# Performance work log

Hardware: AMD Instinct MI355X
Metric: run time of the kernel (lower is better)

## Reference

```python
import jax, jax.numpy as jnp
import numpy as np

B, D, P, C = 4096, 512, 256, 8
LAMBDA = 1.0


def setup_inputs() -> dict:
    key = jax.random.key(0)
    k1, k2, k3, k4 = jax.random.split(key, 4)
    x = jax.random.normal(k1, (B, D), dtype=jnp.float32)
    y = jax.random.randint(k2, (B,), 0, C, dtype=jnp.int32)
    prototypes = jax.random.normal(k3, (P, D), dtype=jnp.float32)
    # omega initialized as eye + 0.01*randn per class, like the torch module
    omega = jnp.eye(D, dtype=jnp.float32)[None] + 0.01 * jax.random.normal(k4, (C, D, D), dtype=jnp.float32)
    prototype_labels = (jnp.arange(P, dtype=jnp.int32) % C).astype(jnp.int32)
    return {"x": x, "y": y, "prototypes": prototypes, "omega": omega, "prototype_labels": prototype_labels}


def reference(x, y, prototypes, omega, prototype_labels):
    # transformed inputs per class: tx[c,b,:] = omega[c] @ x[b]
    tx = jnp.einsum('cij,bj->cbi', omega, x)                     # [C,B,D]
    # transformed prototypes under every class omega, then pick each
    # prototype's own class matrix: tp[p,:] = omega[label[p]] @ w[p]
    tp_all = jnp.einsum('cij,pj->cpi', omega, prototypes)        # [C,P,D]
    tp = tp_all[prototype_labels, jnp.arange(P)]                 # [P,D]
    # squared distances via expansion ||a-b||^2 = |a|^2 + |b|^2 - 2ab
    dots = jnp.einsum('cbd,pd->cbp', tx, tp)                     # [C,B,P]
    x2 = jnp.sum(tx * tx, axis=-1)                               # [C,B]
    p2 = jnp.sum(tp * tp, axis=-1)                               # [P]
    dist_all = x2[:, :, None] + p2[None, None, :] - 2.0 * dots   # [C,B,P]
    # each prototype uses the omega of its own class
    dist = dist_all[prototype_labels, :, jnp.arange(P)].T        # [B,P]
    same = prototype_labels[None, :] == y[:, None]               # [B,P]
    inf = jnp.float32(jnp.inf)
    pos = jnp.min(jnp.where(same, dist, inf), axis=1)            # [B]
    neg = jnp.min(jnp.where(same, inf, dist), axis=1)            # [B]
    mu = (pos - neg) / (pos + neg)
    loss = jnp.mean(jax.nn.sigmoid(LAMBDA * mu))
    loss = loss + 0.01 * jnp.linalg.norm(omega.reshape(-1))
    return loss
```

## Files before the change

### kernel.cpp

```cpp
#include <hip/hip_runtime.h>
#include <math.h>

typedef unsigned short ushort_t;
typedef __attribute__((ext_vector_type(8))) short short8;
typedef __attribute__((ext_vector_type(4))) float f32x4;

#define B_N 4096
#define D_N 512
#define P_N 256
#define C_N 8

#define ACC_OFF   0
#define P2G_OFF   256
#define X2_OFF    1280
#define XB_OFF    132352
#define OMB_OFF   (XB_OFF + B_N*D_N*2)
#define TPG_OFF   (OMB_OFF + C_N*D_N*D_N*2)
#define UG_OFF    (TPG_OFF + P_N*D_N*2)
#define OMBT_OFF  (UG_OFF + P_N*D_N*2)
#define MINB_OFF  OMBT_OFF

#define MFMA16(a, b, c) __builtin_amdgcn_mfma_f32_16x16x32_bf16(a, b, c, 0, 0, 0)

__device__ inline ushort_t f2bf(float f) {
    union { float f; unsigned u; } v; v.f = f;
    unsigned r = v.u + 0x7FFFu + ((v.u >> 16) & 1u);
    return (ushort_t)(r >> 16);
}

__device__ __forceinline__ void gll16(const ushort_t* g, ushort_t* l) {
    __builtin_amdgcn_global_load_lds((const __attribute__((address_space(1))) void*)g,
                                     (__attribute__((address_space(3))) void*)l, 16, 0, 0);
}

__global__ void k_cast(const float* __restrict__ x, const float* __restrict__ omega,
                       ushort_t* __restrict__ xb, ushort_t* __restrict__ omb,
                       ushort_t* __restrict__ ombT, float* __restrict__ oss) {
    __shared__ ushort_t T[64][72];
    __shared__ float red[4];
    int t = threadIdx.x;
    if (blockIdx.x < 1024) {
        int idx = blockIdx.x * 256 + t;
        const float4* x4 = (const float4*)x;
        float4 a = x4[idx * 2], b = x4[idx * 2 + 1];
        union { ushort_t s[8]; uint4 v; } o;
        o.s[0] = f2bf(a.x); o.s[1] = f2bf(a.y); o.s[2] = f2bf(a.z); o.s[3] = f2bf(a.w);
        o.s[4] = f2bf(b.x); o.s[5] = f2bf(b.y); o.s[6] = f2bf(b.z); o.s[7] = f2bf(b.w);
        ((uint4*)xb)[idx] = o.v;
        return;
    }
    int bid = blockIdx.x - 1024;
    int c = bid >> 6, by = (bid >> 3) & 7, bx = bid & 7;
    int r0 = by * 64, c0 = bx * 64;
    int r = t >> 2, seg = t & 3;
    const float* src = omega + ((size_t)c * D_N + r0 + r) * D_N + c0 + seg * 16;
    float4 v0 = ((const float4*)src)[0], v1 = ((const float4*)src)[1];
    float4 v2 = ((const float4*)src)[2], v3 = ((const float4*)src)[3];
    float s = v0.x*v0.x + v0.y*v0.y + v0.z*v0.z + v0.w*v0.w
            + v1.x*v1.x + v1.y*v1.y + v1.z*v1.z + v1.w*v1.w
            + v2.x*v2.x + v2.y*v2.y + v2.z*v2.z + v2.w*v2.w
            + v3.x*v3.x + v3.y*v3.y + v3.z*v3.z + v3.w*v3.w;
    union { ushort_t s[16]; uint4 v[2]; } o;
    float vv[16] = {v0.x,v0.y,v0.z,v0.w, v1.x,v1.y,v1.z,v1.w,
                    v2.x,v2.y,v2.z,v2.w, v3.x,v3.y,v3.z,v3.w};
    #pragma unroll
    for (int j = 0; j < 16; ++j) o.s[j] = f2bf(vv[j]);
    uint4* dst = (uint4*)(omb + ((size_t)c * D_N + r0 + r) * D_N + c0 + seg * 16);
    dst[0] = o.v[0]; dst[1] = o.v[1];
    #pragma unroll
    for (int j = 0; j < 16; ++j) T[seg * 16 + j][r] = o.s[j];
    __syncthreads();
    int jr = t >> 2, sg2 = t & 3;
    uint4 w0 = *(uint4*)&T[jr][sg2 * 16];
    uint4 w1 = *(uint4*)&T[jr][sg2 * 16 + 8];
    uint4* dstT = (uint4*)(ombT + ((size_t)c * D_N + c0 + jr) * D_N + r0 + sg2 * 16);
    dstT[0] = w0; dstT[1] = w1;
    #pragma unroll
    for (int off = 32; off > 0; off >>= 1) s += __shfl_down(s, off);
    if ((t & 63) == 0) red[t >> 6] = s;
    __syncthreads();
    if (t == 0) atomicAdd(oss, red[0] + red[1] + red[2] + red[3]);
}

__global__ __launch_bounds__(256) void k_tp(const float* __restrict__ prot,
                                            const ushort_t* __restrict__ omb,
                                            ushort_t* __restrict__ tpg,
                                            float* __restrict__ p2g) {
    int i0 = blockIdx.x * 64, c = blockIdx.y;
    __shared__ ushort_t As[32][72];
    __shared__ ushort_t Bs[64][72];
    int t = threadIdx.x, w = t >> 6, lane = t & 63;
    int g = lane >> 4, cl = lane & 15;
    f32x4 acc[2] = {{0,0,0,0},{0,0,0,0}};
    for (int k0 = 0; k0 < D_N; k0 += 64) {
        __syncthreads();
        {
            int m = t >> 3, seg = t & 7;
            const float* ap = prot + ((size_t)(c + 8 * m)) * D_N + k0 + seg * 8;
            float4 u0 = ((const float4*)ap)[0], u1 = ((const float4*)ap)[1];
            union { ushort_t s[8]; uint4 v; } o;
            o.s[0]=f2bf(u0.x); o.s[1]=f2bf(u0.y); o.s[2]=f2bf(u0.z); o.s[3]=f2bf(u0.w);
            o.s[4]=f2bf(u1.x); o.s[5]=f2bf(u1.y); o.s[6]=f2bf(u1.z); o.s[7]=f2bf(u1.w);
            *(uint4*)&As[m][seg * 8] = o.v;
        }
        {
            int r = t >> 2, sg = t & 3;
            const uint4* bp = (const uint4*)(omb + ((size_t)c * D_N + i0 + r) * D_N + k0 + sg * 16);
            *(uint4*)&Bs[r][sg * 16] = bp[0];
            *(uint4*)&Bs[r][sg * 16 + 8] = bp[1];
        }
        __syncthreads();
        #pragma unroll
        for (int kk = 0; kk < 2; ++kk) {
            int koff = kk * 32 + g * 8;
            short8 bfr = *(const short8*)&Bs[w * 16 + cl][koff];
            #pragma unroll
            for (int mt = 0; mt < 2; ++mt) {
                short8 afr = *(const short8*)&As[mt * 16 + cl][koff];
                acc[mt] = MFMA16(afr, bfr, acc[mt]);
            }
        }
    }
    #pragma unroll
    for (int mt = 0; mt < 2; ++mt)
        #pragma unroll
        for (int reg = 0; reg < 4; ++reg) {
            float v = acc[mt][reg];
            int m = mt * 16 + g * 4 + reg;
            int i = i0 + w * 16 + cl;
            tpg[((size_t)c * 32 + m) * D_N + i] = f2bf(v);
            float s = v * v;
            s += __shfl_xor(s, 1); s += __shfl_xor(s, 2);
            s += __shfl_xor(s, 4); s += __shfl_xor(s, 8);
            if (cl == 0) atomicAdd(&p2g[c * 32 + m], s);
        }
}

__global__ __launch_bounds__(256) void k_u(const ushort_t* __restrict__ tpg,
                                           const ushort_t* __restrict__ ombT,
                                           ushort_t* __restrict__ ug) {
    int j0 = blockIdx.x * 64, c = blockIdx.y;
    __shared__ ushort_t As[32][72];
    __shared__ ushort_t Bs[64][72];
    int t = threadIdx.x, w = t >> 6, lane = t & 63;
    int g = lane >> 4, cl = lane & 15;
    f32x4 acc[2] = {{0,0,0,0},{0,0,0,0}};
    for (int k0 = 0; k0 < D_N; k0 += 64) {
        __syncthreads();
        {
            int m = t >> 3, seg = t & 7;
            *(uint4*)&As[m][seg * 8] =
                *(const uint4*)(tpg + ((size_t)c * 32 + m) * D_N + k0 + seg * 8);
        }
        {
            int r = t >> 2, sg = t & 3;
            const uint4* bp = (const uint4*)(ombT + ((size_t)c * D_N + j0 + r) * D_N + k0 + sg * 16);
            *(uint4*)&Bs[r][sg * 16] = bp[0];
            *(uint4*)&Bs[r][sg * 16 + 8] = bp[1];
        }
        __syncthreads();
        #pragma unroll
        for (int kk = 0; kk < 2; ++kk) {
            int koff = kk * 32 + g * 8;
            short8 bfr = *(const short8*)&Bs[w * 16 + cl][koff];
            #pragma unroll
            for (int mt = 0; mt < 2; ++mt) {
                short8 afr = *(const short8*)&As[mt * 16 + cl][koff];
                acc[mt] = MFMA16(afr, bfr, acc[mt]);
            }
        }
    }
    #pragma unroll
    for (int mt = 0; mt < 2; ++mt)
        #pragma unroll
        for (int reg = 0; reg < 4; ++reg) {
            int m = mt * 16 + g * 4 + reg;
            int j = j0 + w * 16 + cl;
            ug[((size_t)c * 32 + m) * D_N + j] = f2bf(acc[mt][reg]);
        }
}

__global__ __attribute__((amdgpu_flat_work_group_size(256, 256), amdgpu_waves_per_eu(3, 3)))
void k_x2d(const ushort_t* __restrict__ xb,
           const ushort_t* __restrict__ omb,
           const ushort_t* __restrict__ ug,
           const float* __restrict__ p2g,
           float* __restrict__ x2,
           float* __restrict__ minb) {
    int c  = blockIdx.y;
    int b0 = blockIdx.z * 128;
    int t = threadIdx.x, w = t >> 6, lane = t & 63;
    int g = lane >> 4, cl = lane & 15;
    int srow = lane >> 2, spos = lane & 3;

    __shared__ ushort_t Xs[2][128][32];
    __shared__ ushort_t Os[2][128][32];
    __shared__ float red[128][2];

    if (blockIdx.x < 4) {
        int i0 = blockIdx.x * 128;
        int qr = w >> 1, qc = w & 1;
        f32x4 acc[4][4];
        #pragma unroll
        for (int mt = 0; mt < 4; ++mt)
            #pragma unroll
            for (int nt = 0; nt < 4; ++nt) acc[mt][nt] = (f32x4){0,0,0,0};

        #define STG(bf, k1) do {                                                        \
            _Pragma("unroll")                                                           \
            for (int i = 0; i < 2; ++i) {                                               \
                int rb = w * 32 + i * 16;                                               \
                int r  = rb + srow;                                                     \
                int cg = (spos + r) & 3;                                                \
                gll16(xb + (size_t)(b0 + r) * D_N + (k1) + cg * 8, &Xs[bf][rb][0]);     \
                gll16(omb + ((size_t)c * D_N + i0 + r) * D_N + (k1) + cg * 8,           \
                      &Os[bf][rb][0]);                                                  \
            } } while (0)

        #define CMP(cb) do {                                                            \
            short8 a_[4], b_[4];                                                        \
            _Pragma("unroll")                                                           \
            for (int mt = 0; mt < 4; ++mt) {                                            \
                int r = qr * 64 + mt * 16 + cl;                                         \
                a_[mt] = *(const short8*)&Xs[cb][r][((g - r) & 3) * 8];                 \
            }                                                                           \
            _Pragma("unroll")                                                           \
            for (int nt = 0; nt < 4; ++nt) {                                            \
                int r = qc * 64 + nt * 16 + cl;                                         \
                b_[nt] = *(const short8*)&Os[cb][r][((g - r) & 3) * 8];                 \
            }                                                                           \
            _Pragma("unroll")                                                           \
            for (int mt = 0; mt < 4; ++mt)                                              \
                _Pragma("unroll")                                                       \
                for (int nt = 0; nt < 4; ++nt)                                          \
                    acc[mt][nt] = MFMA16(a_[mt], b_[nt], acc[mt][nt]);                  \
            } while (0)

        STG(0, 0);
        STG(1, 32);
        for (int s = 0; s < 15; ++s) {
            int cb = s & 1;
            asm volatile("s_waitcnt vmcnt(4)" ::: "memory");
            __builtin_amdgcn_s_barrier();
            __builtin_amdgcn_sched_barrier(0);
            CMP(cb);
            __builtin_amdgcn_sched_barrier(0);
            __builtin_amdgcn_s_barrier();
            if (s < 14) STG(cb, (s + 2) * 32);
        }
        asm volatile("s_waitcnt vmcnt(0)" ::: "memory");
        __builtin_amdgcn_s_barrier();
        __builtin_amdgcn_sched_barrier(0);
        CMP(1);
        #undef STG
        #undef CMP
        #pragma unroll
        for (int mt = 0; mt < 4; ++mt)
            #pragma unroll
            for (int reg = 0; reg < 4; ++reg) {
                float s = 0.f;
                #pragma unroll
                for (int nt = 0; nt < 4; ++nt) s += acc[mt][nt][reg] * acc[mt][nt][reg];
                s += __shfl_xor(s, 1); s += __shfl_xor(s, 2);
                s += __shfl_xor(s, 4); s += __shfl_xor(s, 8);
                if (cl == 0) red[qr * 64 + mt * 16 + g * 4 + reg][qc] = s;
            }
        __syncthreads();
        if (t < 128) atomicAdd(&x2[(size_t)(b0 + t) * C_N + c], red[t][0] + red[t][1]);
    } else {
        f32x4 acc[2][2];
        #pragma unroll
        for (int mt = 0; mt < 2; ++mt)
            #pragma unroll
            for (int nt = 0; nt < 2; ++nt) acc[mt][nt] = (f32x4){0,0,0,0};
        #pragma unroll
        for (int i = 0; i < 2; ++i) {
            int rb = w * 32 + i * 16;
            int r  = rb + srow;
            int cg = (spos + r) & 3;
            gll16(xb + (size_t)(b0 + r) * D_N + cg * 8, &Xs[0][rb][0]);
        }
        if (w < 2) {
            int rb = w * 16;
            int r  = rb + srow;
            int cg = (spos + r) & 3;
            gll16(ug + ((size_t)c * 32 + r) * D_N + cg * 8, &Os[0][rb][0]);
        }
        __syncthreads();
        for (int s = 0; s < 16; ++s) {
            int cb = s & 1, nb = cb ^ 1;
            if (s < 15) {
                int k1 = (s + 1) * 32;
                #pragma unroll
                for (int i = 0; i < 2; ++i) {
                    int rb = w * 32 + i * 16;
                    int r  = rb + srow;
                    int cg = (spos + r) & 3;
                    gll16(xb + (size_t)(b0 + r) * D_N + k1 + cg * 8, &Xs[nb][rb][0]);
                }
                if (w < 2) {
                    int rb = w * 16;
                    int r  = rb + srow;
                    int cg = (spos + r) & 3;
                    gll16(ug + ((size_t)c * 32 + r) * D_N + k1 + cg * 8, &Os[nb][rb][0]);
                }
            }
            short8 a[2], b[2];
            #pragma unroll
            for (int mt = 0; mt < 2; ++mt) {
                int r = w * 32 + mt * 16 + cl;
                a[mt] = *(const short8*)&Xs[cb][r][((g - r) & 3) * 8];
            }
            #pragma unroll
            for (int nt = 0; nt < 2; ++nt) {
                int r = nt * 16 + cl;
                b[nt] = *(const short8*)&Os[cb][r][((g - r) & 3) * 8];
            }
            #pragma unroll
            for (int mt = 0; mt < 2; ++mt)
                #pragma unroll
                for (int nt = 0; nt < 2; ++nt)
                    acc[mt][nt] = MFMA16(a[mt], b[nt], acc[mt][nt]);
            __syncthreads();
        }
        #pragma unroll
        for (int mt = 0; mt < 2; ++mt)
            #pragma unroll
            for (int reg = 0; reg < 4; ++reg) {
                float v = INFINITY;
                #pragma unroll
                for (int nt = 0; nt < 2; ++nt) {
                    int q = c * 32 + nt * 16 + cl;
                    v = fminf(v, p2g[q] - 2.f * acc[mt][nt][reg]);
                }
                v = fminf(v, __shfl_xor(v, 1)); v = fminf(v, __shfl_xor(v, 2));
                v = fminf(v, __shfl_xor(v, 4)); v = fminf(v, __shfl_xor(v, 8));
                if (cl == 0)
                    minb[(size_t)(b0 + w * 32 + mt * 16 + g * 4 + reg) * C_N + c] = v;
            }
    }
}

__global__ void k_mu(const float* __restrict__ x2, const float* __restrict__ minb,
                     const int* __restrict__ y, float* __restrict__ accs,
                     float* __restrict__ out) {
    int t = threadIdx.x;
    int b = blockIdx.x * 256 + t;
    int yb = y[b];
    float d[8];
    #pragma unroll
    for (int cc = 0; cc < 8; ++cc)
        d[cc] = x2[(size_t)b * C_N + cc] + minb[(size_t)b * C_N + cc];
    float pos = d[yb];
    float neg = INFINITY;
    #pragma unroll
    for (int cc = 0; cc < 8; ++cc)
        if (cc != yb) neg = fminf(neg, d[cc]);
    float mu = (pos - neg) / (pos + neg);
    float s = 1.f / (1.f + expf(-mu));
    #pragma unroll
    for (int off = 32; off > 0; off >>= 1) s += __shfl_down(s, off);
    __shared__ float red[4];
    if ((t & 63) == 0) red[t >> 6] = s;
    __syncthreads();
    if (t == 0) {
        atomicAdd(accs, red[0] + red[1] + red[2] + red[3]);
        __threadfence();
        unsigned n = atomicAdd((unsigned*)(accs + 2), 1u);
        if (n == (unsigned)(B_N / 256 - 1)) {
            float ls  = atomicAdd(accs, 0.f);
            float oss = atomicAdd(accs + 1, 0.f);
            out[0] = ls * (1.f / (float)B_N) + 0.01f * sqrtf(oss);
        }
    }
}

extern "C" void kernel_launch(void* const* d_in, const int* in_sizes, int n_in,
                              void* d_out, int out_size, void* d_ws, size_t ws_size,
                              hipStream_t stream) {
    (void)in_sizes; (void)n_in; (void)out_size; (void)ws_size;
    const float* x     = (const float*)d_in[0];
    const int*   y     = (const int*)d_in[1];
    const float* prot  = (const float*)d_in[2];
    const float* omega = (const float*)d_in[3];

    char* ws = (char*)d_ws;
    float*    accs = (float*)(ws + ACC_OFF);
    float*    p2g  = (float*)(ws + P2G_OFF);
    float*    x2   = (float*)(ws + X2_OFF);
    ushort_t* xb   = (ushort_t*)(ws + XB_OFF);
    ushort_t* omb  = (ushort_t*)(ws + OMB_OFF);
    ushort_t* tpg  = (ushort_t*)(ws + TPG_OFF);
    ushort_t* ug   = (ushort_t*)(ws + UG_OFF);
    ushort_t* ombT = (ushort_t*)(ws + OMBT_OFF);
    float*    minb = (float*)(ws + MINB_OFF);

    (void)hipMemsetAsync(ws, 0, XB_OFF, stream);
    k_cast <<<1536, 256, 0, stream>>>(x, omega, xb, omb, ombT, accs + 1);
    k_tp   <<<dim3(8, C_N), 256, 0, stream>>>(prot, omb, tpg, p2g);
    k_u    <<<dim3(8, C_N), 256, 0, stream>>>(tpg, ombT, ug);
    k_x2d  <<<dim3(5, C_N, B_N / 128), 256, 0, stream>>>(xb, omb, ug, p2g, x2, minb);
    k_mu   <<<B_N / 256, 256, 0, stream>>>(x2, minb, y, accs, (float*)d_out);
}
```

Before: 130.4 us.

## Fuse launches: fold memset into cast, merge tp/u, fold mu reduction into x2d

Cuts five launches plus a memset down to three kernels. The workspace zeroing moves into extra blocks of the cast kernel. The tp and u GEMMs are merged into one kernel where u blocks spin on a per-class counter until the tp blocks finish. The final mu/sigmoid reduction runs in the last-arriving block per batch tile of the distance kernel, using ticket counters and a last-block final sum. The aim is to remove launch gaps and tail latency, in exchange for spin-wait dependence on co-residency and a more complex ordering scheme built on fences.

```diff
diff --git a/kernel.cpp b/kernel.cpp
--- a/kernel.cpp
+++ b/kernel.cpp
@@ -10,10 +10,15 @@
 #define P_N 256
 #define C_N 8
 
-#define ACC_OFF   0
+#define TK_OFF    0
+#define TTK_OFF   64
+#define FTK_OFF   192
 #define P2G_OFF   256
 #define X2_OFF    1280
-#define XB_OFF    132352
+#define ZERO_BYTES 132352
+#define OSSP_OFF  132352
+#define MUSUM_OFF 134400
+#define XB_OFF    135168
 #define OMB_OFF   (XB_OFF + B_N*D_N*2)
 #define TPG_OFF   (OMB_OFF + C_N*D_N*D_N*2)
 #define UG_OFF    (TPG_OFF + P_N*D_N*2)
@@ -35,10 +40,18 @@
 
 __global__ void k_cast(const float* __restrict__ x, const float* __restrict__ omega,
                        ushort_t* __restrict__ xb, ushort_t* __restrict__ omb,
-                       ushort_t* __restrict__ ombT, float* __restrict__ oss) {
+                       ushort_t* __restrict__ ombT, float* __restrict__ ossp,
+                       char* __restrict__ zbase) {
     __shared__ ushort_t T[64][72];
     __shared__ float red[4];
     int t = threadIdx.x;
+    if (blockIdx.x >= 1536) {
+        int zb = blockIdx.x - 1536;
+        uint4 z4 = {0, 0, 0, 0};
+        for (size_t off = ((size_t)zb * 256 + t) * 16; off < (size_t)ZERO_BYTES; off += 8u * 256u * 16u)
+            *(uint4*)(zbase + off) = z4;
+        return;
+    }
     if (blockIdx.x < 1024) {
         int idx = blockIdx.x * 256 + t;
         const float4* x4 = (const float4*)x;
@@ -79,116 +92,127 @@
     for (int off = 32; off > 0; off >>= 1) s += __shfl_down(s, off);
     if ((t & 63) == 0) red[t >> 6] = s;
     __syncthreads();
-    if (t == 0) atomicAdd(oss, red[0] + red[1] + red[2] + red[3]);
-}
-
-__global__ __launch_bounds__(256) void k_tp(const float* __restrict__ prot,
-                                            const ushort_t* __restrict__ omb,
-                                            ushort_t* __restrict__ tpg,
-                                            float* __restrict__ p2g) {
-    int i0 = blockIdx.x * 64, c = blockIdx.y;
+    if (t == 0) ossp[bid] = red[0] + red[1] + red[2] + red[3];
+}
+
+__global__ __launch_bounds__(256) void k_tpu(const float* __restrict__ prot,
+                                             const ushort_t* __restrict__ omb,
+                                             const ushort_t* __restrict__ ombT,
+                                             ushort_t* __restrict__ tpg,
+                                             ushort_t* __restrict__ ug,
+                                             float* __restrict__ p2g,
+                                             unsigned* __restrict__ tk) {
     __shared__ ushort_t As[32][72];
     __shared__ ushort_t Bs[64][72];
+    int bid = blockIdx.x;
     int t = threadIdx.x, w = t >> 6, lane = t & 63;
     int g = lane >> 4, cl = lane & 15;
     f32x4 acc[2] = {{0,0,0,0},{0,0,0,0}};
-    for (int k0 = 0; k0 < D_N; k0 += 64) {
-        __syncthreads();
-        {
-            int m = t >> 3, seg = t & 7;
-            const float* ap = prot + ((size_t)(c + 8 * m)) * D_N + k0 + seg * 8;
-            float4 u0 = ((const float4*)ap)[0], u1 = ((const float4*)ap)[1];
-            union { ushort_t s[8]; uint4 v; } o;
-            o.s[0]=f2bf(u0.x); o.s[1]=f2bf(u0.y); o.s[2]=f2bf(u0.z); o.s[3]=f2bf(u0.w);
-            o.s[4]=f2bf(u1.x); o.s[5]=f2bf(u1.y); o.s[6]=f2bf(u1.z); o.s[7]=f2bf(u1.w);
-            *(uint4*)&As[m][seg * 8] = o.v;
-        }
-        {
-            int r = t >> 2, sg = t & 3;
-            const uint4* bp = (const uint4*)(omb + ((size_t)c * D_N + i0 + r) * D_N + k0 + sg * 16);
-            *(uint4*)&Bs[r][sg * 16] = bp[0];
-            *(uint4*)&Bs[r][sg * 16 + 8] = bp[1];
-        }
-        __syncthreads();
-        #pragma unroll
-        for (int kk = 0; kk < 2; ++kk) {
-            int koff = kk * 32 + g * 8;
-            short8 bfr = *(const short8*)&Bs[w * 16 + cl][koff];
-            #pragma unroll
-            for (int mt = 0; mt < 2; ++mt) {
-                short8 afr = *(const short8*)&As[mt * 16 + cl][koff];
-                acc[mt] = MFMA16(afr, bfr, acc[mt]);
-            }
-        }
-    }
-    #pragma unroll
-    for (int mt = 0; mt < 2; ++mt)
-        #pragma unroll
-        for (int reg = 0; reg < 4; ++reg) {
-            float v = acc[mt][reg];
-            int m = mt * 16 + g * 4 + reg;
-            int i = i0 + w * 16 + cl;
-            tpg[((size_t)c * 32 + m) * D_N + i] = f2bf(v);
-            float s = v * v;
-            s += __shfl_xor(s, 1); s += __shfl_xor(s, 2);
-            s += __shfl_xor(s, 4); s += __shfl_xor(s, 8);
-            if (cl == 0) atomicAdd(&p2g[c * 32 + m], s);
-        }
-}
-
-__global__ __launch_bounds__(256) void k_u(const ushort_t* __restrict__ tpg,
-                                           const ushort_t* __restrict__ ombT,
-                                           ushort_t* __restrict__ ug) {
-    int j0 = blockIdx.x * 64, c = blockIdx.y;
-    __shared__ ushort_t As[32][72];
-    __shared__ ushort_t Bs[64][72];
-    int t = threadIdx.x, w = t >> 6, lane = t & 63;
-    int g = lane >> 4, cl = lane & 15;
-    f32x4 acc[2] = {{0,0,0,0},{0,0,0,0}};
-    for (int k0 = 0; k0 < D_N; k0 += 64) {
-        __syncthreads();
-        {
-            int m = t >> 3, seg = t & 7;
-            *(uint4*)&As[m][seg * 8] =
-                *(const uint4*)(tpg + ((size_t)c * 32 + m) * D_N + k0 + seg * 8);
-        }
-        {
-            int r = t >> 2, sg = t & 3;
-            const uint4* bp = (const uint4*)(ombT + ((size_t)c * D_N + j0 + r) * D_N + k0 + sg * 16);
-            *(uint4*)&Bs[r][sg * 16] = bp[0];
-            *(uint4*)&Bs[r][sg * 16 + 8] = bp[1];
-        }
-        __syncthreads();
-        #pragma unroll
-        for (int kk = 0; kk < 2; ++kk) {
-            int koff = kk * 32 + g * 8;
-            short8 bfr = *(const short8*)&Bs[w * 16 + cl][koff];
-            #pragma unroll
-            for (int mt = 0; mt < 2; ++mt) {
-                short8 afr = *(const short8*)&As[mt * 16 + cl][koff];
-                acc[mt] = MFMA16(afr, bfr, acc[mt]);
-            }
-        }
-    }
-    #pragma unroll
-    for (int mt = 0; mt < 2; ++mt)
-        #pragma unroll
-        for (int reg = 0; reg < 4; ++reg) {
-            int m = mt * 16 + g * 4 + reg;
-            int j = j0 + w * 16 + cl;
-            ug[((size_t)c * 32 + m) * D_N + j] = f2bf(acc[mt][reg]);
-        }
+    if (bid < 64) {
+        int c = bid >> 3, i0 = (bid & 7) * 64;
+        for (int k0 = 0; k0 < D_N; k0 += 64) {
+            __syncthreads();
+            {
+                int m = t >> 3, seg = t & 7;
+                const float* ap = prot + ((size_t)(c + 8 * m)) * D_N + k0 + seg * 8;
+                float4 u0 = ((const float4*)ap)[0], u1 = ((const float4*)ap)[1];
+                union { ushort_t s[8]; uint4 v; } o;
+                o.s[0]=f2bf(u0.x); o.s[1]=f2bf(u0.y); o.s[2]=f2bf(u0.z); o.s[3]=f2bf(u0.w);
+                o.s[4]=f2bf(u1.x); o.s[5]=f2bf(u1.y); o.s[6]=f2bf(u1.z); o.s[7]=f2bf(u1.w);
+                *(uint4*)&As[m][seg * 8] = o.v;
+            }
+            {
+                int r = t >> 2, sg = t & 3;
+                const uint4* bp = (const uint4*)(omb + ((size_t)c * D_N + i0 + r) * D_N + k0 + sg * 16);
+                *(uint4*)&Bs[r][sg * 16] = bp[0];
+                *(uint4*)&Bs[r][sg * 16 + 8] = bp[1];
+            }
+            __syncthreads();
+            #pragma unroll
+            for (int kk = 0; kk < 2; ++kk) {
+                int koff = kk * 32 + g * 8;
+                short8 bfr = *(const short8*)&Bs[w * 16 + cl][koff];
+                #pragma unroll
+                for (int mt = 0; mt < 2; ++mt) {
+                    short8 afr = *(const short8*)&As[mt * 16 + cl][koff];
+                    acc[mt] = MFMA16(afr, bfr, acc[mt]);
+                }
+            }
+        }
+        #pragma unroll
+        for (int mt = 0; mt < 2; ++mt)
+            #pragma unroll
+            for (int reg = 0; reg < 4; ++reg) {
+                float v = acc[mt][reg];
+                int m = mt * 16 + g * 4 + reg;
+                int i = i0 + w * 16 + cl;
+                tpg[((size_t)c * 32 + m) * D_N + i] = f2bf(v);
+                float s = v * v;
+                s += __shfl_xor(s, 1); s += __shfl_xor(s, 2);
+                s += __shfl_xor(s, 4); s += __shfl_xor(s, 8);
+                if (cl == 0) atomicAdd(&p2g[c * 32 + m], s);
+            }
+        __syncthreads();
+        if (t == 0) { __threadfence(); atomicAdd(&tk[c], 1u); }
+    } else {
+        int u = bid - 64, c = u >> 3, j0 = (u & 7) * 64;
+        if (t == 0) {
+            while (atomicAdd(&tk[c], 0u) < 8u) __builtin_amdgcn_s_sleep(8);
+            __threadfence();
+        }
+        __syncthreads();
+        for (int k0 = 0; k0 < D_N; k0 += 64) {
+            __syncthreads();
+            {
+                int m = t >> 3, seg = t & 7;
+                *(uint4*)&As[m][seg * 8] =
+                    *(const uint4*)(tpg + ((size_t)c * 32 + m) * D_N + k0 + seg * 8);
+            }
+            {
+                int r = t >> 2, sg = t & 3;
+                const uint4* bp = (const uint4*)(ombT + ((size_t)c * D_N + j0 + r) * D_N + k0 + sg * 16);
+                *(uint4*)&Bs[r][sg * 16] = bp[0];
+                *(uint4*)&Bs[r][sg * 16 + 8] = bp[1];
+            }
+            __syncthreads();
+            #pragma unroll
+            for (int kk = 0; kk < 2; ++kk) {
+                int koff = kk * 32 + g * 8;
+                short8 bfr = *(const short8*)&Bs[w * 16 + cl][koff];
+                #pragma unroll
+                for (int mt = 0; mt < 2; ++mt) {
+                    short8 afr = *(const short8*)&As[mt * 16 + cl][koff];
+                    acc[mt] = MFMA16(afr, bfr, acc[mt]);
+                }
+            }
+        }
+        #pragma unroll
+        for (int mt = 0; mt < 2; ++mt)
+            #pragma unroll
+            for (int reg = 0; reg < 4; ++reg) {
+                int m = mt * 16 + g * 4 + reg;
+                int j = j0 + w * 16 + cl;
+                ug[((size_t)c * 32 + m) * D_N + j] = f2bf(acc[mt][reg]);
+            }
+    }
 }
 
 __global__ __attribute__((amdgpu_flat_work_group_size(256, 256), amdgpu_waves_per_eu(3, 3)))
-void k_x2d(const ushort_t* __restrict__ xb,
-           const ushort_t* __restrict__ omb,
-           const ushort_t* __restrict__ ug,
-           const float* __restrict__ p2g,
-           float* __restrict__ x2,
-           float* __restrict__ minb) {
+void k_x2dm(const ushort_t* __restrict__ xb,
+            const ushort_t* __restrict__ omb,
+            const ushort_t* __restrict__ ug,
+            const float* __restrict__ p2g,
+            float* __restrict__ x2,
+            float* __restrict__ minb,
+            const int* __restrict__ y,
+            const float* __restrict__ ossp,
+            float* __restrict__ musum,
+            unsigned* __restrict__ ttk,
+            unsigned* __restrict__ ftk,
+            float* __restrict__ out) {
     int c  = blockIdx.y;
-    int b0 = blockIdx.z * 128;
+    int z  = blockIdx.z;
+    int b0 = z * 128;
     int t = threadIdx.x, w = t >> 6, lane = t & 63;
     int g = lane >> 4, cl = lane & 15;
     int srow = lane >> 2, spos = lane & 3;
@@ -196,6 +220,8 @@
     __shared__ ushort_t Xs[2][128][32];
     __shared__ ushort_t Os[2][128][32];
     __shared__ float red[128][2];
+    __shared__ float rr[4], rr2[4];
+    __shared__ bool flg1, flg2;
 
     if (blockIdx.x < 4) {
         int i0 = blockIdx.x * 128;
@@ -339,38 +365,55 @@
                     minb[(size_t)(b0 + w * 32 + mt * 16 + g * 4 + reg) * C_N + c] = v;
             }
     }
-}
-
-__global__ void k_mu(const float* __restrict__ x2, const float* __restrict__ minb,
-                     const int* __restrict__ y, float* __restrict__ accs,
-                     float* __restrict__ out) {
-    int t = threadIdx.x;
-    int b = blockIdx.x * 256 + t;
-    int yb = y[b];
-    float d[8];
-    #pragma unroll
-    for (int cc = 0; cc < 8; ++cc)
-        d[cc] = x2[(size_t)b * C_N + cc] + minb[(size_t)b * C_N + cc];
-    float pos = d[yb];
-    float neg = INFINITY;
-    #pragma unroll
-    for (int cc = 0; cc < 8; ++cc)
-        if (cc != yb) neg = fminf(neg, d[cc]);
-    float mu = (pos - neg) / (pos + neg);
-    float s = 1.f / (1.f + expf(-mu));
-    #pragma unroll
-    for (int off = 32; off > 0; off >>= 1) s += __shfl_down(s, off);
-    __shared__ float red[4];
-    if ((t & 63) == 0) red[t >> 6] = s;
+
     __syncthreads();
     if (t == 0) {
-        atomicAdd(accs, red[0] + red[1] + red[2] + red[3]);
         __threadfence();
-        unsigned n = atomicAdd((unsigned*)(accs + 2), 1u);
-        if (n == (unsigned)(B_N / 256 - 1)) {
-            float ls  = atomicAdd(accs, 0.f);
-            float oss = atomicAdd(accs + 1, 0.f);
-            out[0] = ls * (1.f / (float)B_N) + 0.01f * sqrtf(oss);
+        unsigned o = atomicAdd(&ttk[z], 1u);
+        flg1 = (o == 39u);
+        if (flg1) __threadfence();
+    }
+    __syncthreads();
+    if (flg1) {
+        float s = 0.f;
+        if (t < 128) {
+            int b = b0 + t, yb = y[b];
+            float pos = 0.f, neg = INFINITY;
+            #pragma unroll
+            for (int cc = 0; cc < 8; ++cc) {
+                float dd = x2[(size_t)b * C_N + cc] + minb[(size_t)b * C_N + cc];
+                if (cc == yb) pos = dd; else neg = fminf(neg, dd);
+            }
+            float mu = (pos - neg) / (pos + neg);
+            s = 1.f / (1.f + expf(-mu));
+        }
+        #pragma unroll
+        for (int off = 32; off > 0; off >>= 1) s += __shfl_down(s, off);
+        if ((t & 63) == 0) rr[t >> 6] = s;
+        __syncthreads();
+        if (t == 0) {
+            musum[z] = rr[0] + rr[1] + rr[2] + rr[3];
+            __threadfence();
+            unsigned o2 = atomicAdd(ftk, 1u);
+            flg2 = (o2 == 31u);
+            if (flg2) __threadfence();
+        }
+        __syncthreads();
+        if (flg2) {
+            float a1 = (t < 32) ? musum[t] : 0.f;
+            float a2 = ossp[2 * t] + ossp[2 * t + 1];
+            #pragma unroll
+            for (int off = 32; off > 0; off >>= 1) {
+                a1 += __shfl_down(a1, off);
+                a2 += __shfl_down(a2, off);
+            }
+            if ((t & 63) == 0) { rr[t >> 6] = a1; rr2[t >> 6] = a2; }
+            __syncthreads();
+            if (t == 0) {
+                float ls  = rr[0] + rr[1] + rr[2] + rr[3];
+                float oss = rr2[0] + rr2[1] + rr2[2] + rr2[3];
+                out[0] = ls * (1.f / (float)B_N) + 0.01f * sqrtf(oss);
+            }
         }
     }
 }
@@ -385,20 +428,23 @@
     const float* omega = (const float*)d_in[3];
 
     char* ws = (char*)d_ws;
-    float*    accs = (float*)(ws + ACC_OFF);
-    float*    p2g  = (float*)(ws + P2G_OFF);
-    float*    x2   = (float*)(ws + X2_OFF);
-    ushort_t* xb   = (ushort_t*)(ws + XB_OFF);
-    ushort_t* omb  = (ushort_t*)(ws + OMB_OFF);
-    ushort_t* tpg  = (ushort_t*)(ws + TPG_OFF);
-    ushort_t* ug   = (ushort_t*)(ws + UG_OFF);
-    ushort_t* ombT = (ushort_t*)(ws + OMBT_OFF);
-    float*    minb = (float*)(ws + MINB_OFF);
-
-    (void)hipMemsetAsync(ws, 0, XB_OFF, stream);
-    k_cast <<<1536, 256, 0, stream>>>(x, omega, xb, omb, ombT, accs + 1);
-    k_tp   <<<dim3(8, C_N), 256, 0, stream>>>(prot, omb, tpg, p2g);
-    k_u    <<<dim3(8, C_N), 256, 0, stream>>>(tpg, ombT, ug);
-    k_x2d  <<<dim3(5, C_N, B_N / 128), 256, 0, stream>>>(xb, omb, ug, p2g, x2, minb);
-    k_mu   <<<B_N / 256, 256, 0, stream>>>(x2, minb, y, accs, (float*)d_out);
-}
+    unsigned* tk    = (unsigned*)(ws + TK_OFF);
+    unsigned* ttk   = (unsigned*)(ws + TTK_OFF);
+    unsigned* ftk   = (unsigned*)(ws + FTK_OFF);
+    float*    p2g   = (float*)(ws + P2G_OFF);
+    float*    x2    = (float*)(ws + X2_OFF);
+    float*    ossp  = (float*)(ws + OSSP_OFF);
+    float*    musum = (float*)(ws + MUSUM_OFF);
+    ushort_t* xb    = (ushort_t*)(ws + XB_OFF);
+    ushort_t* omb   = (ushort_t*)(ws + OMB_OFF);
+    ushort_t* tpg   = (ushort_t*)(ws + TPG_OFF);
+    ushort_t* ug    = (ushort_t*)(ws + UG_OFF);
+    ushort_t* ombT  = (ushort_t*)(ws + OMBT_OFF);
+    float*    minb  = (float*)(ws + MINB_OFF);
+
+    k_cast <<<1544, 256, 0, stream>>>(x, omega, xb, omb, ombT, ossp, ws);
+    k_tpu  <<<128, 256, 0, stream>>>(prot, omb, ombT, tpg, ug, p2g, tk);
+    k_x2dm <<<dim3(5, C_N, B_N / 128), 256, 0, stream>>>(xb, omb, ug, p2g, x2, minb,
+                                                         y, ossp, musum, ttk, ftk,
+                                                         (float*)d_out);
+}
```

Result: slower. 152.5 us (+16.9%).
